# Optimization experiments

Hardware: AMD Instinct MI355X
Metric: run time of the kernel (lower is better)

Reference implementation:

```python
import jax, jax.numpy as jnp
import numpy as np
from jax import lax

NPOINT = 1024   # FPS centroids
NSAMPLE = 32    # neighbors per ball
RADIUS = 0.1    # ball-query radius (points live in unit cube)


def farthest_point_sample(pos, npoint):
    # pos: [B, N, 3] -> idx [B, npoint] int32
    B, N, _ = pos.shape

    def step(carry, _):
        min_d, far = carry                                   # [B,N], [B]
        centroid = jnp.take_along_axis(pos, far[:, None, None], axis=1)  # [B,1,3]
        d = jnp.sum((pos - centroid) ** 2, axis=-1)          # [B,N]
        min_d = jnp.minimum(min_d, d)
        nxt = jnp.argmax(min_d, axis=1).astype(jnp.int32)
        return (min_d, nxt), far

    init = (jnp.full((B, N), 1e10, pos.dtype), jnp.zeros((B,), jnp.int32))
    _, idx = lax.scan(step, init, None, length=npoint)
    return idx.T                                             # [B, npoint]


def ball_query(new_pos, pos, radius, k):
    # new_pos: [B,M,3], pos: [B,N,3] -> idx [B,M,k] int32
    d2 = (jnp.sum(new_pos ** 2, -1)[:, :, None]
          + jnp.sum(pos ** 2, -1)[:, None, :]
          - 2.0 * jnp.einsum('bmc,bnc->bmn', new_pos, pos))  # [B,M,N]
    neg = jnp.where(d2 <= radius * radius, -d2, -jnp.inf)
    vals, idx = lax.top_k(neg, k)                            # k nearest inside ball
    valid = vals > -jnp.inf
    idx = jnp.where(valid, idx, idx[..., :1])                # replicate first hit (centroid itself)
    return idx.astype(jnp.int32)


def setup_inputs() -> dict:
    key = jax.random.key(0)
    ks = jax.random.split(key, 6)
    B, N, C = 4, 16384, 1
    pos = jax.random.uniform(ks[0], (B, N, 3), dtype=jnp.float32)
    x = jax.random.normal(ks[1], (B, N, C), dtype=jnp.float32)
    c_in = 3 + C  # rel-xyz concat features
    W1 = jax.random.normal(ks[2], (c_in, 32), jnp.float32) * np.sqrt(2.0 / c_in)
    W2 = jax.random.normal(ks[3], (32, 32), jnp.float32) * np.sqrt(2.0 / 32)
    W3 = jax.random.normal(ks[4], (32, 32), jnp.float32) * np.sqrt(2.0 / 32)
    b1 = jnp.zeros((32,), jnp.float32)
    b2 = jnp.zeros((32,), jnp.float32)
    b3 = jnp.zeros((32,), jnp.float32)
    return {"pos": pos, "x": x, "W1": W1, "b1": b1, "W2": W2, "b2": b2, "W3": W3, "b3": b3}


def reference(pos, x, W1, b1, W2, b2, W3, b3):
    # PointNet++ set-abstraction: FPS -> ball query -> group -> shared MLP -> max-pool.
    fps_idx = farthest_point_sample(lax.stop_gradient(pos), NPOINT)       # [B,M]
    new_pos = jnp.take_along_axis(pos, fps_idx[..., None], axis=1)        # [B,M,3]
    idx = ball_query(lax.stop_gradient(new_pos), lax.stop_gradient(pos), RADIUS, NSAMPLE)  # [B,M,K]
    B, M, K = idx.shape
    flat = idx.reshape(B, M * K)
    gpos = jnp.take_along_axis(pos, flat[..., None], axis=1).reshape(B, M, K, 3)
    gx = jnp.take_along_axis(x, flat[..., None], axis=1).reshape(B, M, K, -1)
    rel = gpos - new_pos[:, :, None, :]                                   # local coords
    h = jnp.concatenate([rel, gx], axis=-1)                               # [B,M,K,4]
    h = jax.nn.relu(h @ W1 + b1)
    h = jax.nn.relu(h @ W2 + b2)
    h = jax.nn.relu(h @ W3 + b3)
    return jnp.max(h, axis=2)                                             # [B,M,32]
```

## Files before the change

### kernel.cpp

```cpp
#include <hip/hip_runtime.h>

#define NB 4
#define NPT 16384
#define NPOINT 1024
#define NSAMPLE 32

#define FPS_T 512
#define FPS_PPT (NPT / FPS_T)

#define BQ_WAVES 4
#define CAP 896

__global__ __launch_bounds__(FPS_T, 2) void fps_kernel(
    const float* __restrict__ pos, float* __restrict__ new_pos) {
#pragma clang fp contract(off)
  const int b = blockIdx.x;
  const int tid = threadIdx.x;
  const int wid = tid >> 6;
  const int lane = tid & 63;
  const float* __restrict__ p = pos + (size_t)b * NPT * 3;

  float px[FPS_PPT], py[FPS_PPT], pz[FPS_PPT], md[FPS_PPT];

  {
    const float4* pf4 = (const float4*)(p + (size_t)tid * (FPS_PPT * 3));
#pragma unroll
    for (int k = 0; k < FPS_PPT / 4; ++k) {
      const float4 a = pf4[3 * k + 0];
      const float4 bq = pf4[3 * k + 1];
      const float4 c = pf4[3 * k + 2];
      px[4 * k + 0] = a.x; py[4 * k + 0] = a.y; pz[4 * k + 0] = a.z;
      px[4 * k + 1] = a.w; py[4 * k + 1] = bq.x; pz[4 * k + 1] = bq.y;
      px[4 * k + 2] = bq.z; py[4 * k + 2] = bq.w; pz[4 * k + 2] = c.x;
      px[4 * k + 3] = c.y; py[4 * k + 3] = c.z; pz[4 * k + 3] = c.w;
    }
#pragma unroll
    for (int i = 0; i < FPS_PPT; ++i) md[i] = 1e10f;
  }

  __shared__ unsigned long long red[3];
  if (tid < 3) red[tid] = 0ull;
  __syncthreads();

  float cx = p[0], cy = p[1], cz = p[2];

  for (int j = 0; j < NPOINT; ++j) {
    if (tid == 0) {
      float* q = new_pos + ((size_t)b * NPOINT + j) * 3;
      q[0] = cx;
      q[1] = cy;
      q[2] = cz;
    }
    float bm = -1.0f;
    int bi = 0;
#pragma unroll
    for (int i = 0; i < FPS_PPT; ++i) {
      const float dx = px[i] - cx;
      const float dy = py[i] - cy;
      const float dz = pz[i] - cz;
      const float d = (dx * dx + dy * dy) + dz * dz;
      const float m = fminf(md[i], d);
      md[i] = m;
      if (m > bm) {
        bm = m;
        bi = i;
      }
    }
    float wm = bm;
#pragma unroll
    for (int off = 1; off < 64; off <<= 1)
      wm = fmaxf(wm, __shfl_xor(wm, off, 64));
    const unsigned long long tied = __ballot(bm == wm);
    const int wl = __ffsll((long long)tied) - 1;
    const int wbi = __shfl(bi, wl, 64);
    const int widx = ((wid << 6) + wl) * FPS_PPT + wbi;
    if (lane == 0) {
      const unsigned long long key =
          ((unsigned long long)__float_as_uint(wm) << 32) |
          (unsigned)(~widx);
      atomicMax(&red[j % 3], key);
    }
    __syncthreads();
    const unsigned long long w = red[j % 3];
    if (tid == 0) red[(j + 2) % 3] = 0ull;
    const int nf = (int)(~(unsigned)w);
    cx = p[nf * 3 + 0];
    cy = p[nf * 3 + 1];
    cz = p[nf * 3 + 2];
  }
}

__global__ __launch_bounds__(256) void bq_mlp_kernel(
    const float* __restrict__ pos, const float* __restrict__ x,
    const float* __restrict__ W1, const float* __restrict__ b1,
    const float* __restrict__ W2, const float* __restrict__ b2,
    const float* __restrict__ W3, const float* __restrict__ b3,
    const float* __restrict__ new_pos, float* __restrict__ out) {
#pragma clang fp contract(off)
  __shared__ __align__(16) float w1s[4 * 32];
  __shared__ __align__(16) float w2s[32 * 32];
  __shared__ __align__(16) float w3s[32 * 32];
  __shared__ float b1s[32], b2s[32], b3s[32];
  __shared__ unsigned long long list[BQ_WAVES][CAP];
  __shared__ int sel[BQ_WAVES][NSAMPLE];
  __shared__ unsigned cnt[BQ_WAVES];

  const int tid = threadIdx.x;
  const int wid = tid >> 6;
  const int lane = tid & 63;

  for (int i = tid; i < 128; i += 256) w1s[i] = W1[i];
  for (int i = tid; i < 1024; i += 256) {
    w2s[i] = W2[i];
    w3s[i] = W3[i];
  }
  if (tid < 32) {
    b1s[tid] = b1[tid];
    b2s[tid] = b2[tid];
    b3s[tid] = b3[tid];
  }
  if (lane == 0) cnt[wid] = 0u;
  __syncthreads();

  const int m_global = blockIdx.x * BQ_WAVES + wid;
  const int b = m_global >> 10;
  const float* __restrict__ p = pos + (size_t)b * NPT * 3;
  const float* __restrict__ xb = x + (size_t)b * NPT;

  const float cx = new_pos[(size_t)m_global * 3 + 0];
  const float cy = new_pos[(size_t)m_global * 3 + 1];
  const float cz = new_pos[(size_t)m_global * 3 + 2];
  const float snew = (cx * cx + cy * cy) + cz * cz;

  for (int it = 0; it < NPT / 256; ++it) {
    const int n0 = it * 256 + lane * 4;
    const float4* pf4 = (const float4*)(p + (size_t)n0 * 3);
    const float4 a = pf4[0];
    const float4 bq = pf4[1];
    const float4 c = pf4[2];
    float qx[4], qy[4], qz[4];
    qx[0] = a.x;  qy[0] = a.y;  qz[0] = a.z;
    qx[1] = a.w;  qy[1] = bq.x; qz[1] = bq.y;
    qx[2] = bq.z; qy[2] = bq.w; qz[2] = c.x;
    qx[3] = c.y;  qy[3] = c.z;  qz[3] = c.w;
#pragma unroll
    for (int t = 0; t < 4; ++t) {
      const float spos = (qx[t] * qx[t] + qy[t] * qy[t]) + qz[t] * qz[t];
      const float dot = (cx * qx[t] + cy * qy[t]) + cz * qz[t];
      const float d2 = (snew + spos) - 2.0f * dot;
      if (d2 <= 0.01f) {
        const unsigned u = __float_as_uint(d2);
        const unsigned key = (u & 0x80000000u) ? ~u : (u | 0x80000000u);
        const unsigned li = atomicAdd(&cnt[wid], 1u);
        if (li < CAP)
          list[wid][li] = ((unsigned long long)key << 32) | (unsigned)(n0 + t);
      }
    }
  }
  __syncthreads();

  int c = (int)cnt[wid];
  if (c > CAP) c = CAP;
  const int nsel = c < NSAMPLE ? c : NSAMPLE;

  for (int i = lane; i < c; i += 64) {
    const unsigned long long ki = list[wid][i];
    int rank = 0;
    for (int jj = 0; jj < c; ++jj) rank += (list[wid][jj] < ki) ? 1 : 0;
    if (rank < NSAMPLE) sel[wid][rank] = (int)(unsigned)(ki & 0xFFFFFFFFull);
  }
  __syncthreads();

  const bool active = (lane < nsel);
  const int n = sel[wid][active ? lane : 0];

  const float gpx = p[n * 3 + 0];
  const float gpy = p[n * 3 + 1];
  const float gpz = p[n * 3 + 2];
  const float gxv = xb[n];

  const float h0 = gpx - cx, h1i = gpy - cy, h2i = gpz - cz, h3i = gxv;

  float h1[32];
#pragma unroll
  for (int o = 0; o < 32; ++o) {
    float a = b1s[o];
    a += h0 * w1s[0 * 32 + o];
    a += h1i * w1s[1 * 32 + o];
    a += h2i * w1s[2 * 32 + o];
    a += h3i * w1s[3 * 32 + o];
    h1[o] = fmaxf(a, 0.0f);
  }

  float acc[32];
#pragma unroll
  for (int o = 0; o < 32; ++o) acc[o] = b2s[o];
  for (int k = 0; k < 32; ++k) {
    const float hk = h1[k];
    const float4* row = (const float4*)&w2s[k * 32];
#pragma unroll
    for (int q = 0; q < 8; ++q) {
      const float4 ww = row[q];
      acc[4 * q + 0] += hk * ww.x;
      acc[4 * q + 1] += hk * ww.y;
      acc[4 * q + 2] += hk * ww.z;
      acc[4 * q + 3] += hk * ww.w;
    }
  }
#pragma unroll
  for (int o = 0; o < 32; ++o) h1[o] = fmaxf(acc[o], 0.0f);

#pragma unroll
  for (int o = 0; o < 32; ++o) acc[o] = b3s[o];
  for (int k = 0; k < 32; ++k) {
    const float hk = h1[k];
    const float4* row = (const float4*)&w3s[k * 32];
#pragma unroll
    for (int q = 0; q < 8; ++q) {
      const float4 ww = row[q];
      acc[4 * q + 0] += hk * ww.x;
      acc[4 * q + 1] += hk * ww.y;
      acc[4 * q + 2] += hk * ww.z;
      acc[4 * q + 3] += hk * ww.w;
    }
  }
#pragma unroll
  for (int o = 0; o < 32; ++o)
    acc[o] = active ? fmaxf(acc[o], 0.0f) : -INFINITY;

#pragma unroll
  for (int mask = 1; mask <= 16; mask <<= 1) {
#pragma unroll
    for (int o = 0; o < 32; ++o)
      acc[o] = fmaxf(acc[o], __shfl_xor(acc[o], mask, 64));
  }

  if (lane == 0) {
    float4* o4 = (float4*)(out + (size_t)m_global * 32);
#pragma unroll
    for (int q = 0; q < 8; ++q)
      o4[q] = make_float4(acc[4 * q + 0], acc[4 * q + 1], acc[4 * q + 2],
                          acc[4 * q + 3]);
  }
}

extern "C" void kernel_launch(void* const* d_in, const int* in_sizes, int n_in,
                              void* d_out, int out_size, void* d_ws,
                              size_t ws_size, hipStream_t stream) {
  const float* pos = (const float*)d_in[0];
  const float* x = (const float*)d_in[1];
  const float* W1 = (const float*)d_in[2];
  const float* b1 = (const float*)d_in[3];
  const float* W2 = (const float*)d_in[4];
  const float* b2 = (const float*)d_in[5];
  const float* W3 = (const float*)d_in[6];
  const float* b3 = (const float*)d_in[7];
  float* out = (float*)d_out;
  float* new_pos = (float*)d_ws;

  fps_kernel<<<NB, FPS_T, 0, stream>>>(pos, new_pos);
  bq_mlp_kernel<<<(NB * NPOINT) / BQ_WAVES, 256, 0, stream>>>(
      pos, x, W1, b1, W2, b2, W3, b3, new_pos, out);
}
```

Measured before the change: 1.906 ms.

## Morton-sort FPS points and skip groups via bounding-sphere pruning

Farthest point sampling now bins points into an 8x8x8 Morton grid and counting-sorts them in LDS, so each wave owns spatially coherent groups of 256 points. Each group gets a bounding sphere and a running max of min-distances, which lets whole groups be skipped when the new centroid cannot lower any of their distances. Reductions switch from shuffles to DPP, the next centroid is read from LDS instead of global memory, and centroid outputs are buffered in LDS and written once at the end. This adds setup cost, heavy LDS use, and a more involved tie-breaking scheme that must still select the lowest original index.

```diff
diff --git a/kernel.cpp b/kernel.cpp
--- a/kernel.cpp
+++ b/kernel.cpp
@@ -6,12 +6,44 @@
 #define NSAMPLE 32
 
 #define FPS_T 512
-#define FPS_PPT (NPT / FPS_T)
 
 #define BQ_WAVES 4
 #define CAP 896
 
-__global__ __launch_bounds__(FPS_T, 2) void fps_kernel(
+template <int CTRL>
+__device__ __forceinline__ float dpp_fmax(float v) {
+  const int s =
+      __builtin_amdgcn_update_dpp(0, __float_as_int(v), CTRL, 0xf, 0xf, true);
+  return fmaxf(v, __int_as_float(s));
+}
+template <int CTRL>
+__device__ __forceinline__ float dpp_fmin(float v) {
+  const int s = __builtin_amdgcn_update_dpp(__float_as_int(v),
+                                            __float_as_int(v), CTRL, 0xf, 0xf,
+                                            false);
+  const float o = __int_as_float(s);
+  return fminf(v, o);
+}
+template <int CTRL>
+__device__ __forceinline__ unsigned dpp_umin(unsigned v) {
+  const unsigned s = (unsigned)__builtin_amdgcn_update_dpp((int)v, (int)v,
+                                                           CTRL, 0xf, 0xf,
+                                                           false);
+  return s < v ? s : v;
+}
+#define DPP_CHAIN(fn, v)                                                      \
+  v = fn<0x111>(v);                                           \
+  v = fn<0x112>(v);                                           \
+  v = fn<0x114>(v);                                           \
+  v = fn<0x118>(v);                                           \
+  v = fn<0x142>(v);                                         \
+  v = fn<0x143>(v);
+
+__device__ __forceinline__ unsigned part3(unsigned v) {
+  return (v & 1u) | ((v & 2u) << 2) | ((v & 4u) << 4);
+}
+
+__global__ __launch_bounds__(FPS_T) void fps_kernel(
     const float* __restrict__ pos, float* __restrict__ new_pos) {
 #pragma clang fp contract(off)
   const int b = blockIdx.x;
@@ -20,74 +52,186 @@
   const int lane = tid & 63;
   const float* __restrict__ p = pos + (size_t)b * NPT * 3;
 
-  float px[FPS_PPT], py[FPS_PPT], pz[FPS_PPT], md[FPS_PPT];
-
+  __shared__ __align__(16) unsigned char lds[131072 + 1024 + 256 + 12288 + 32 + 96];
+  float2* sxy = (float2*)lds;
+  unsigned* sidx = (unsigned*)lds;
+  unsigned* hist = (unsigned*)(lds + 65536);
+  unsigned* cursor = (unsigned*)(lds + 65536 + 2048);
+  float4* gbox = (float4*)(lds + 131072);
+  float* gmd = (float*)(lds + 131072 + 1024);
+  float* clog = (float*)(lds + 131072 + 1024 + 256);
+  unsigned long long* red =
+      (unsigned long long*)(lds + 131072 + 1024 + 256 + 12288);
+  float* wzs = (float*)(lds + 131072 + 1024 + 256 + 12288 + 32);
+
+  hist[tid] = 0u;
+  __syncthreads();
+  unsigned mort[32];
   {
-    const float4* pf4 = (const float4*)(p + (size_t)tid * (FPS_PPT * 3));
-#pragma unroll
-    for (int k = 0; k < FPS_PPT / 4; ++k) {
-      const float4 a = pf4[3 * k + 0];
-      const float4 bq = pf4[3 * k + 1];
-      const float4 c = pf4[3 * k + 2];
-      px[4 * k + 0] = a.x; py[4 * k + 0] = a.y; pz[4 * k + 0] = a.z;
-      px[4 * k + 1] = a.w; py[4 * k + 1] = bq.x; pz[4 * k + 1] = bq.y;
-      px[4 * k + 2] = bq.z; py[4 * k + 2] = bq.w; pz[4 * k + 2] = c.x;
-      px[4 * k + 3] = c.y; py[4 * k + 3] = c.z; pz[4 * k + 3] = c.w;
-    }
-#pragma unroll
-    for (int i = 0; i < FPS_PPT; ++i) md[i] = 1e10f;
-  }
-
-  __shared__ unsigned long long red[3];
+    const float4* pf4 = (const float4*)(p + (size_t)tid * 96);
+    float Xt[32], Yt[32], Zt[32];
+#pragma unroll
+    for (int k = 0; k < 8; ++k) {
+      const float4 A = pf4[3 * k + 0];
+      const float4 B = pf4[3 * k + 1];
+      const float4 C = pf4[3 * k + 2];
+      Xt[4 * k + 0] = A.x; Yt[4 * k + 0] = A.y; Zt[4 * k + 0] = A.z;
+      Xt[4 * k + 1] = A.w; Yt[4 * k + 1] = B.x; Zt[4 * k + 1] = B.y;
+      Xt[4 * k + 2] = B.z; Yt[4 * k + 2] = B.w; Zt[4 * k + 2] = C.x;
+      Xt[4 * k + 3] = C.y; Yt[4 * k + 3] = C.z; Zt[4 * k + 3] = C.w;
+    }
+#pragma unroll
+    for (int i = 0; i < 32; ++i) {
+      int gx = (int)(Xt[i] * 8.0f); gx = gx > 7 ? 7 : (gx < 0 ? 0 : gx);
+      int gy = (int)(Yt[i] * 8.0f); gy = gy > 7 ? 7 : (gy < 0 ? 0 : gy);
+      int gz = (int)(Zt[i] * 8.0f); gz = gz > 7 ? 7 : (gz < 0 ? 0 : gz);
+      mort[i] = part3((unsigned)gx) | (part3((unsigned)gy) << 1) |
+                (part3((unsigned)gz) << 2);
+      atomicAdd(&hist[mort[i]], 1u);
+    }
+  }
+  __syncthreads();
+  cursor[tid] = hist[tid];
+  __syncthreads();
+  for (int d = 1; d < 512; d <<= 1) {
+    const unsigned v = (tid >= d) ? cursor[tid - d] : 0u;
+    __syncthreads();
+    cursor[tid] += v;
+    __syncthreads();
+  }
+  cursor[tid] -= hist[tid];
+  __syncthreads();
+#pragma unroll
+  for (int i = 0; i < 32; ++i) {
+    const unsigned slot = atomicAdd(&cursor[mort[i]], 1u);
+    sidx[slot] = (unsigned)(tid * 32 + i);
+  }
+  __syncthreads();
+  const int base_sp = wid * 2048 + lane;
+  unsigned IDX[32];
+#pragma unroll
+  for (int g = 0; g < 8; ++g)
+#pragma unroll
+    for (int s = 0; s < 4; ++s)
+      IDX[g * 4 + s] = sidx[base_sp + g * 256 + s * 64];
+  __syncthreads();
+  float Zc[32], Xs[32], Ys[32];
+#pragma unroll
+  for (int g = 0; g < 8; ++g)
+#pragma unroll
+    for (int s = 0; s < 4; ++s) {
+      const unsigned oi = IDX[g * 4 + s];
+      const float x = p[oi * 3 + 0];
+      const float y = p[oi * 3 + 1];
+      const float z = p[oi * 3 + 2];
+      Xs[g * 4 + s] = x; Ys[g * 4 + s] = y; Zc[g * 4 + s] = z;
+      sxy[base_sp + g * 256 + s * 64] = make_float2(x, y);
+    }
+#pragma unroll
+  for (int g = 0; g < 8; ++g) {
+    float mnx = fminf(fminf(Xs[g * 4], Xs[g * 4 + 1]), fminf(Xs[g * 4 + 2], Xs[g * 4 + 3]));
+    float mxx = fmaxf(fmaxf(Xs[g * 4], Xs[g * 4 + 1]), fmaxf(Xs[g * 4 + 2], Xs[g * 4 + 3]));
+    float mny = fminf(fminf(Ys[g * 4], Ys[g * 4 + 1]), fminf(Ys[g * 4 + 2], Ys[g * 4 + 3]));
+    float mxy = fmaxf(fmaxf(Ys[g * 4], Ys[g * 4 + 1]), fmaxf(Ys[g * 4 + 2], Ys[g * 4 + 3]));
+    float mnz = fminf(fminf(Zc[g * 4], Zc[g * 4 + 1]), fminf(Zc[g * 4 + 2], Zc[g * 4 + 3]));
+    float mxz = fmaxf(fmaxf(Zc[g * 4], Zc[g * 4 + 1]), fmaxf(Zc[g * 4 + 2], Zc[g * 4 + 3]));
+    DPP_CHAIN(dpp_fmin, mnx) DPP_CHAIN(dpp_fmax, mxx)
+    DPP_CHAIN(dpp_fmin, mny) DPP_CHAIN(dpp_fmax, mxy)
+    DPP_CHAIN(dpp_fmin, mnz) DPP_CHAIN(dpp_fmax, mxz)
+    if (lane == 63) {
+      const float ex = mxx - mnx, ey = mxy - mny, ez = mxz - mnz;
+      const float r = 0.5f * sqrtf(ex * ex + ey * ey + ez * ez) + 1e-4f;
+      gbox[wid * 8 + g] =
+          make_float4(0.5f * (mnx + mxx), 0.5f * (mny + mxy), 0.5f * (mnz + mxz), r);
+      gmd[wid * 8 + g] = 1e10f;
+    }
+  }
   if (tid < 3) red[tid] = 0ull;
   __syncthreads();
+
+  float md[32];
+#pragma unroll
+  for (int i = 0; i < 32; ++i) md[i] = 1e10f;
+  float m4[8], z4[8];
+  unsigned c4[8];
+#pragma unroll
+  for (int g = 0; g < 8; ++g) { m4[g] = -1.0f; c4[g] = 0u; z4[g] = 0.0f; }
 
   float cx = p[0], cy = p[1], cz = p[2];
 
   for (int j = 0; j < NPOINT; ++j) {
     if (tid == 0) {
-      float* q = new_pos + ((size_t)b * NPOINT + j) * 3;
-      q[0] = cx;
-      q[1] = cy;
-      q[2] = cz;
-    }
-    float bm = -1.0f;
-    int bi = 0;
-#pragma unroll
-    for (int i = 0; i < FPS_PPT; ++i) {
-      const float dx = px[i] - cx;
-      const float dy = py[i] - cy;
-      const float dz = pz[i] - cz;
-      const float d = (dx * dx + dy * dy) + dz * dz;
-      const float m = fminf(md[i], d);
-      md[i] = m;
-      if (m > bm) {
-        bm = m;
-        bi = i;
+      clog[3 * j + 0] = cx;
+      clog[3 * j + 1] = cy;
+      clog[3 * j + 2] = cz;
+    }
+#pragma unroll
+    for (int g = 0; g < 8; ++g) {
+      const float4 bb = gbox[wid * 8 + g];
+      const float gm = gmd[wid * 8 + g];
+      const float ddx = bb.x - cx, ddy = bb.y - cy, ddz = bb.z - cz;
+      const float q = ddx * ddx + ddy * ddy + ddz * ddz;
+      const float t = sqrtf(q) - bb.w;
+      const int skip = (t > 0.0f) && (t * t >= gm);
+      if (!__builtin_amdgcn_readfirstlane(skip)) {
+        float gmv = -1.0f, gz = 0.0f;
+        unsigned gc = 0u;
+#pragma unroll
+        for (int s = 0; s < 4; ++s) {
+          const float2 xy = sxy[base_sp + g * 256 + s * 64];
+          const float dx = xy.x - cx;
+          const float dy = xy.y - cy;
+          const float dz = Zc[g * 4 + s] - cz;
+          const float d = (dx * dx + dy * dy) + dz * dz;
+          const float m = fminf(md[g * 4 + s], d);
+          md[g * 4 + s] = m;
+          if (m > gmv) {
+            gmv = m;
+            gc = (IDX[g * 4 + s] << 14) | (unsigned)(base_sp + g * 256 + s * 64);
+            gz = Zc[g * 4 + s];
+          }
+        }
+        m4[g] = gmv; c4[g] = gc; z4[g] = gz;
+        float wmx = gmv;
+        DPP_CHAIN(dpp_fmax, wmx)
+        if (lane == 63) gmd[wid * 8 + g] = wmx;
       }
     }
-    float wm = bm;
-#pragma unroll
-    for (int off = 1; off < 64; off <<= 1)
-      wm = fmaxf(wm, __shfl_xor(wm, off, 64));
-    const unsigned long long tied = __ballot(bm == wm);
-    const int wl = __ffsll((long long)tied) - 1;
-    const int wbi = __shfl(bi, wl, 64);
-    const int widx = ((wid << 6) + wl) * FPS_PPT + wbi;
+    float bm = m4[0], bz = z4[0];
+    unsigned bc = c4[0];
+#pragma unroll
+    for (int g = 1; g < 8; ++g)
+      if (m4[g] > bm) { bm = m4[g]; bc = c4[g]; bz = z4[g]; }
+    float v = bm;
+    DPP_CHAIN(dpp_fmax, v)
+    const float wm =
+        __int_as_float(__builtin_amdgcn_readlane(__float_as_int(v), 63));
+    unsigned cand = (bm == wm) ? bc : 0x0FFFFFFFu;
+    DPP_CHAIN(dpp_umin, cand)
+    const unsigned wc = (unsigned)__builtin_amdgcn_readlane((int)cand, 63);
+    const unsigned long long tl = __ballot(bm == wm && bc == wc);
+    const int wl = __ffsll((long long)tl) - 1;
+    const float wbz =
+        __int_as_float(__builtin_amdgcn_readlane(__float_as_int(bz), wl));
     if (lane == 0) {
-      const unsigned long long key =
-          ((unsigned long long)__float_as_uint(wm) << 32) |
-          (unsigned)(~widx);
-      atomicMax(&red[j % 3], key);
+      atomicMax(&red[j % 3],
+                ((unsigned long long)__float_as_uint(wm) << 32) | (unsigned)(~wc));
+      wzs[(j % 3) * 8 + wid] = wbz;
     }
     __syncthreads();
     const unsigned long long w = red[j % 3];
     if (tid == 0) red[(j + 2) % 3] = 0ull;
-    const int nf = (int)(~(unsigned)w);
-    cx = p[nf * 3 + 0];
-    cy = p[nf * 3 + 1];
-    cz = p[nf * 3 + 2];
-  }
+    const unsigned wca = ~(unsigned)w;
+    const unsigned sp = wca & 0x3FFFu;
+    cz = wzs[(j % 3) * 8 + (sp >> 11)];
+    const float2 cxy = sxy[sp];
+    cx = cxy.x;
+    cy = cxy.y;
+  }
+
+  __syncthreads();
+  for (int k = tid; k < NPOINT * 3; k += FPS_T)
+    new_pos[(size_t)b * NPOINT * 3 + k] = clog[k];
 }
 
 __global__ __launch_bounds__(256) void bq_mlp_kernel(
```

Measured after the change: 3.164 ms. 1.66x slower.
